# Performance work log

Measured on AMD Instinct MI355X. Metric: run time of the kernel, lower is better.

## Reference

```python
import jax, jax.numpy as jnp
import numpy as np

B, C, H, W, D = 4, 256, 16, 16, 16
N = H * W * D          # 4096 tokens == input_size
HEADS, P = 8, 64       # num_heads, proj_size
EPS_LN, EPS_BN, NEG_SLOPE = 1e-5, 1e-5, 0.01


def setup_inputs() -> dict:
    key = jax.random.key(0)
    ks = jax.random.split(key, 10)
    s = 0.02
    rn = lambda k, shp: (s * jax.random.normal(k, shp)).astype(jnp.float32)
    return {
        "x": jax.random.normal(ks[0], (B, C, H, W, D), jnp.float32),
        "gamma": 1e-6 * jnp.ones((C,), jnp.float32),
        "ln_w": jnp.ones((C,), jnp.float32),
        "ln_b": jnp.zeros((C,), jnp.float32),
        "qkvv_w": rn(ks[1], (4 * C, C)),          # Linear(C, 4C), bias=False
        "ef_w": rn(ks[2], (P, N)),                 # shared E == F projection
        "ef_b": jnp.zeros((P,), jnp.float32),
        "temp": jnp.ones((HEADS, 1, 1), jnp.float32),
        "temp2": jnp.ones((HEADS, 1, 1), jnp.float32),
        "op1_w": rn(ks[3], (C // 2, C)),
        "op1_b": jnp.zeros((C // 2,), jnp.float32),
        "op2_w": rn(ks[4], (C // 2, C)),
        "op2_b": jnp.zeros((C // 2,), jnp.float32),
        "conv1_w": rn(ks[5], (C, C, 3, 3, 3)),     # UnetResBlock convs, bias=False
        "bn1_w": jnp.ones((C,), jnp.float32),
        "bn1_b": jnp.zeros((C,), jnp.float32),
        "conv2_w": rn(ks[6], (C, C, 3, 3, 3)),
        "bn2_w": jnp.ones((C,), jnp.float32),
        "bn2_b": jnp.zeros((C,), jnp.float32),
        "conv8_w": rn(ks[7], (C, C, 1, 1, 1)),     # nn.Conv3d 1x1x1, bias=True
        "conv8_b": jnp.zeros((C,), jnp.float32),
    }


def _l2norm(t):  # torch F.normalize(dim=-1)
    n = jnp.sqrt(jnp.sum(t * t, axis=-1, keepdims=True))
    return t / jnp.maximum(n, 1e-12)


def _conv3d(x, w, pad):
    return jax.lax.conv_general_dilated(
        x, w, window_strides=(1, 1, 1), padding=[(pad, pad)] * 3,
        dimension_numbers=("NCDHW", "OIDHW", "NCDHW"))


def _bn(x, w, b):  # BatchNorm3d, training-mode batch stats, biased var
    mu = jnp.mean(x, axis=(0, 2, 3, 4), keepdims=True)
    var = jnp.mean((x - mu) ** 2, axis=(0, 2, 3, 4), keepdims=True)
    xh = (x - mu) / jnp.sqrt(var + EPS_BN)
    return xh * w[None, :, None, None, None] + b[None, :, None, None, None]


def _lrelu(x):
    return jnp.where(x >= 0, x, NEG_SLOPE * x)


def _epa(xs, qkvv_w, ef_w, ef_b, temp, temp2, op1_w, op1_b, op2_w, op2_b):
    Bq, Nq, Cq = xs.shape
    d = Cq // HEADS
    qkvv = (xs @ qkvv_w.T).reshape(Bq, Nq, 4, HEADS, d)
    qkvv = jnp.transpose(qkvv, (2, 0, 3, 1, 4))         # (4,B,h,N,d)
    q, k, v_ca, v_sa = qkvv[0], qkvv[1], qkvv[2], qkvv[3]
    q = jnp.swapaxes(q, -2, -1)                          # (B,h,d,N)
    k = jnp.swapaxes(k, -2, -1)
    v_ca = jnp.swapaxes(v_ca, -2, -1)
    v_sa = jnp.swapaxes(v_sa, -2, -1)
    k_proj = k @ ef_w.T + ef_b                           # (B,h,d,P)
    v_sa_proj = v_sa @ ef_w.T + ef_b                     # (B,h,d,P)
    qn = _l2norm(q)
    kn = _l2norm(k)
    # channel attention: (B,h,d,d)
    attn_ca = jax.nn.softmax(jnp.einsum("bhdn,bhen->bhde", qn, kn) * temp, axis=-1)
    x_ca = jnp.einsum("bhde,bhen->bhdn", attn_ca, v_ca)  # (B,h,d,N)
    x_ca = jnp.transpose(x_ca, (0, 3, 1, 2)).reshape(Bq, Nq, Cq)
    # spatial attention with projected K/V: (B,h,N,P)
    attn_sa = jax.nn.softmax(jnp.einsum("bhdn,bhdp->bhnp", qn, k_proj) * temp2, axis=-1)
    x_sa = jnp.einsum("bhnp,bhdp->bhnd", attn_sa, v_sa_proj)   # (B,h,N,d)
    # faithful to source: permute(0,3,1,2) then reshape(B,N,C)
    x_sa = jnp.transpose(x_sa, (0, 3, 1, 2)).reshape(Bq, Nq, Cq)
    x_sa = x_sa @ op1_w.T + op1_b
    x_ca = x_ca @ op2_w.T + op2_b
    return jnp.concatenate((x_sa, x_ca), axis=-1)


def reference(x, gamma, ln_w, ln_b, qkvv_w, ef_w, ef_b, temp, temp2,
              op1_w, op1_b, op2_w, op2_b, conv1_w, bn1_w, bn1_b,
              conv2_w, bn2_w, bn2_b, conv8_w, conv8_b):
    Bq, Cq, Hq, Wq, Dq = x.shape
    Nq = Hq * Wq * Dq
    xs = jnp.transpose(x.reshape(Bq, Cq, Nq), (0, 2, 1))       # (B,N,C)
    mu = jnp.mean(xs, axis=-1, keepdims=True)
    var = jnp.mean((xs - mu) ** 2, axis=-1, keepdims=True)
    xn = (xs - mu) / jnp.sqrt(var + EPS_LN) * ln_w + ln_b
    attn = xs + gamma * _epa(xn, qkvv_w, ef_w, ef_b, temp, temp2,
                             op1_w, op1_b, op2_w, op2_b)
    attn_skip = jnp.transpose(attn.reshape(Bq, Hq, Wq, Dq, Cq), (0, 4, 1, 2, 3))
    # UnetResBlock (identity shortcut: same channels, stride 1)
    h1 = _lrelu(_bn(_conv3d(attn_skip, conv1_w, 1), bn1_w, bn1_b))
    h2 = _bn(_conv3d(h1, conv2_w, 1), bn2_w, bn2_b)
    conv_out = _lrelu(h2 + attn_skip)
    # conv8: Dropout3d (identity in eval) + 1x1x1 conv with bias
    c8 = _conv3d(conv_out, conv8_w, 0) + conv8_b[None, :, None, None, None]
    return attn_skip + c8
```

## Files before the change

kernel.cpp:

```cpp
#include <hip/hip_runtime.h>

#define B_ 4
#define C_ 256
#define N_ 4096

typedef unsigned short u16;
typedef __attribute__((ext_vector_type(8))) short short8_t;
typedef __attribute__((ext_vector_type(4))) float f32x4;

__device__ __forceinline__ u16 bf16r(float f) {
  unsigned u = __float_as_uint(f);
  return (u16)((u + 0x7FFFu + ((u >> 16) & 1u)) >> 16);
}
__device__ __forceinline__ float bf2f(u16 u) {
  return __uint_as_float(((unsigned)u) << 16);
}

__device__ __forceinline__ void g2l16(const u16* g, u16* l) {
  __builtin_amdgcn_global_load_lds((const __attribute__((address_space(1))) void*)g,
                                   (__attribute__((address_space(3))) void*)l, 16, 0, 0);
}

__device__ __forceinline__ int f4(int x) { return (x ^ (x >> 2)) & 3; }

__global__ __launch_bounds__(256) void k_pre_ln(const float* __restrict__ x,
                                                const float* __restrict__ ln_w,
                                                const float* __restrict__ ln_b,
                                                const float* __restrict__ qkvv_w,
                                                const float* __restrict__ conv8_w,
                                                const float* __restrict__ op1_w,
                                                const float* __restrict__ op2_w,
                                                const float* __restrict__ ef_w,
                                                const float* __restrict__ conv1_w,
                                                const float* __restrict__ conv2_w,
                                                u16* __restrict__ xnb,
                                                u16* __restrict__ qpack,
                                                u16* __restrict__ w8pack,
                                                u16* __restrict__ oppack,
                                                u16* __restrict__ efpack,
                                                u16* __restrict__ apack1,
                                                u16* __restrict__ apack2,
                                                float* __restrict__ zbuf) {
  __shared__ float tile[32][260];
  __shared__ float s_mu[32], s_rs[32];
  int bid = blockIdx.x, tid = threadIdx.x;
  if (bid < 96) {
    const float* w; u16* dst; int tile_;
    if (bid < 64)      { w = qkvv_w;  dst = qpack;          tile_ = bid; }
    else if (bid < 80) { w = conv8_w; dst = w8pack;         tile_ = bid - 64; }
    else if (bid < 88) { w = op1_w;   dst = oppack;         tile_ = bid - 80; }
    else               { w = op2_w;   dst = oppack + 32768; tile_ = bid - 88; }
    int k0 = tile_ & 7, ot = tile_ >> 3;
    u16* td = dst + (size_t)tile_ * 4096;
    int m = tid >> 1, kb = (tid & 1) * 16, fm = f4(m);
    #pragma unroll
    for (int j = 0; j < 16; ++j) {
      int k = kb + j;
      float v = w[(size_t)(ot * 128 + m) * 256 + k0 * 32 + k];
      td[m * 32 + (((k >> 3) ^ fm) << 3) + (k & 7)] = bf16r(v);
    }
  } else if (bid < 224) {
    int k0 = bid - 96;
    int m = tid & 63, kq = tid >> 6, fm = f4(m);
    u16* td = efpack + (size_t)k0 * 2048;
    #pragma unroll
    for (int kk = 0; kk < 8; ++kk) {
      int k = kq * 8 + kk;
      td[m * 32 + (((k >> 3) ^ fm) << 3) + (k & 7)] = bf16r(ef_w[(size_t)m * 4096 + k0 * 32 + k]);
    }
  } else if (bid < 1088) {
    int t = bid - 224;
    const float* w = (t < 432) ? conv1_w : conv2_w;
    u16* dst = (t < 432) ? apack1 : apack2;
    int tile_ = (t < 432) ? t : t - 432;
    int tap = tile_ % 27; int tmp = tile_ / 27;
    int k0 = tmp & 7; int ot = tmp >> 3;
    u16* td = dst + (size_t)tile_ * 4096;
    int m = tid >> 1, kb = (tid & 1) * 16;
    #pragma unroll
    for (int j = 0; j < 16; ++j) {
      int k = kb + j;
      float v = w[((size_t)(ot * 128 + m) * 256 + k0 * 32 + k) * 27 + tap];
      td[m * 32 + k] = bf16r(v);
    }
  } else if (bid < 1600) {
    int lb = bid - 1088;
    int b = lb >> 7, n0 = (lb & 127) * 32;
    for (int idx = tid; idx < 32 * 256; idx += 256) {
      int nl = idx & 31, c = idx >> 5;
      tile[nl][c] = x[((size_t)(b * C_ + c)) * N_ + n0 + nl];
    }
    __syncthreads();
    int token = tid >> 3, sub = tid & 7;
    float s = 0.f, sq = 0.f;
    for (int j = 0; j < 32; ++j) {
      float v = tile[token][sub + j * 8];
      s += v; sq += v * v;
    }
    for (int o = 1; o < 8; o <<= 1) { s += __shfl_xor(s, o); sq += __shfl_xor(sq, o); }
    if (sub == 0) {
      float mu = s * (1.f / 256.f);
      float var = sq * (1.f / 256.f) - mu * mu;
      s_mu[token] = mu;
      s_rs[token] = rsqrtf(var + 1e-5f);
    }
    __syncthreads();
    int c = tid;
    float lw = ln_w[c], lb2 = ln_b[c];
    for (int k = 0; k < 32; ++k) {
      float v = (tile[k][c] - s_mu[k]) * s_rs[k] * lw + lb2;
      xnb[((size_t)(b * N_ + n0 + k)) * 256 + c] = bf16r(v);
    }
  } else {
    for (int i = tid; i < 3200; i += 256) zbuf[i] = 0.f;
  }
}

__global__ __launch_bounds__(256) void k_gemm(const u16* __restrict__ xnb,
                                              const u16* __restrict__ qpack,
                                              u16* __restrict__ qct,
                                              float* __restrict__ sbuf) {
  __shared__ alignas(16) u16 At[4096];
  __shared__ alignas(16) u16 Bt[4096];
  __shared__ alignas(16) u16 Tt[128 * 136];
  int tid = threadIdx.x, l = tid & 63, w = tid >> 6;
  int wm = w >> 1, wn = w & 1;
  int kg = l >> 4;
  int tok0 = blockIdx.x * 128, oct = blockIdx.y;
  int b = tok0 >> 12;
  int aoff[4], boff[4];
  #pragma unroll
  for (int r = 0; r < 4; ++r) {
    int m = wm * 64 + r * 16 + (l & 15);
    aoff[r] = m * 32 + ((kg ^ f4(m)) << 3);
    int o = wn * 64 + r * 16 + (l & 15);
    boff[r] = o * 32 + ((kg ^ f4(o)) << 3);
  }
  f32x4 acc[4][4];
  #pragma unroll
  for (int r = 0; r < 4; ++r)
    #pragma unroll
    for (int jt = 0; jt < 4; ++jt)
      acc[r][jt] = (f32x4){0.f, 0.f, 0.f, 0.f};
  for (int k0 = 0; k0 < 8; ++k0) {
    __syncthreads();
    #pragma unroll
    for (int it = 0; it < 2; ++it) {
      int slot = it * 256 + tid;
      int row = slot >> 2, cp = slot & 3;
      int cig = cp ^ f4(row);
      g2l16(xnb + ((size_t)(tok0 + row) * 256 + k0 * 32 + cig * 8),
            &At[(it * 256 + (tid & 192)) * 8]);
    }
    const u16* qb = qpack + ((size_t)(oct * 8 + k0) << 12);
    #pragma unroll
    for (int it = 0; it < 2; ++it)
      g2l16(qb + (it * 256 + tid) * 8, &Bt[(it * 256 + (tid & 192)) * 8]);
    __syncthreads();
    short8_t av[4], bv[4];
    #pragma unroll
    for (int r = 0; r < 4; ++r) av[r] = *(const short8_t*)&At[aoff[r]];
    #pragma unroll
    for (int jt = 0; jt < 4; ++jt) bv[jt] = *(const short8_t*)&Bt[boff[jt]];
    #pragma unroll
    for (int r = 0; r < 4; ++r)
      #pragma unroll
      for (int jt = 0; jt < 4; ++jt)
        acc[r][jt] = __builtin_amdgcn_mfma_f32_16x16x32_bf16(av[r], bv[jt], acc[r][jt], 0, 0, 0);
  }
  if (oct < 4) {
    #pragma unroll
    for (int jt = 0; jt < 4; ++jt) {
      float ss = 0.f;
      #pragma unroll
      for (int r = 0; r < 4; ++r)
        #pragma unroll
        for (int reg = 0; reg < 4; ++reg)
          ss += acc[r][jt][reg] * acc[r][jt][reg];
      ss += __shfl_xor(ss, 16);
      ss += __shfl_xor(ss, 32);
      if ((l >> 4) == 0) {
        int oc = oct * 128 + wn * 64 + jt * 16 + (l & 15);
        atomicAdd(&sbuf[(oc >> 8) * 1024 + b * 256 + (oc & 255)], ss);
      }
    }
  }
  #pragma unroll
  for (int r = 0; r < 4; ++r) {
    int tokl = wm * 64 + r * 16 + ((l >> 4) << 2);
    #pragma unroll
    for (int jt = 0; jt < 4; ++jt) {
      int ocl = wn * 64 + jt * 16 + (l & 15);
      ushort4 h4;
      h4.x = bf16r(acc[r][jt][0]);
      h4.y = bf16r(acc[r][jt][1]);
      h4.z = bf16r(acc[r][jt][2]);
      h4.w = bf16r(acc[r][jt][3]);
      *(ushort4*)&Tt[ocl * 136 + tokl] = h4;
    }
  }
  __syncthreads();
  int n0 = tok0 & 4095;
  #pragma unroll
  for (int i = 0; i < 8; ++i) {
    int s = i * 256 + tid;
    int row = s >> 4;
    int col = (s & 15) * 8;
    *(int4*)&qct[((size_t)(b * 1024 + oct * 128 + row)) * 4096 + n0 + col] =
        *(const int4*)&Tt[row * 136 + col];
  }
}

__global__ __launch_bounds__(256) void k_kvproj_m(const u16* __restrict__ qct,
                                                  const u16* __restrict__ efp,
                                                  float* __restrict__ kvpart) {
  __shared__ alignas(16) u16 At[16384];
  __shared__ alignas(16) u16 Bt[8192];
  int tid = threadIdx.x, l = tid & 63, w = tid >> 6;
  int mt = blockIdx.x, b = blockIdx.y, kz = blockIdx.z;
  int ccb = (mt < 2) ? (256 + mt * 128) : (768 + (mt - 2) * 128);
  int kg = l >> 4;
  int aoff[2], boff[4];
  #pragma unroll
  for (int r = 0; r < 2; ++r) {
    int m = w * 32 + r * 16 + (l & 15);
    aoff[r] = m * 32 + ((kg ^ f4(m)) << 3);
  }
  #pragma unroll
  for (int jt = 0; jt < 4; ++jt) {
    int o = jt * 16 + (l & 15);
    boff[jt] = o * 32 + ((kg ^ f4(o)) << 3);
  }
  f32x4 acc[2][4];
  #pragma unroll
  for (int r = 0; r < 2; ++r)
    #pragma unroll
    for (int jt = 0; jt < 4; ++jt) acc[r][jt] = (f32x4){0.f, 0.f, 0.f, 0.f};
  for (int k0 = kz * 8; k0 < kz * 8 + 8; ++k0) {
    __syncthreads();
    #pragma unroll
    for (int it = 0; it < 8; ++it) {
      int slot = it * 256 + tid;
      int sub = slot >> 9, r = (slot >> 2) & 127, cp = slot & 3;
      g2l16(qct + ((size_t)(b * 1024 + ccb + r)) * 4096 + k0 * 128 + sub * 32 + ((cp ^ f4(r)) << 3),
            &At[(it * 256 + (tid & 192)) * 8]);
    }
    #pragma unroll
    for (int it = 0; it < 4; ++it) {
      int slot = it * 256 + tid;
      g2l16(efp + (size_t)k0 * 8192 + slot * 8, &Bt[(it * 256 + (tid & 192)) * 8]);
    }
    __syncthreads();
    #pragma unroll
    for (int sub = 0; sub < 4; ++sub) {
      short8_t av[2], bv[4];
      #pragma unroll
      for (int r = 0; r < 2; ++r) av[r] = *(const short8_t*)&At[sub * 4096 + aoff[r]];
      #pragma unroll
      for (int jt = 0; jt < 4; ++jt) bv[jt] = *(const short8_t*)&Bt[sub * 2048 + boff[jt]];
      #pragma unroll
      for (int r = 0; r < 2; ++r)
        #pragma unroll
        for (int jt = 0; jt < 4; ++jt)
          acc[r][jt] = __builtin_amdgcn_mfma_f32_16x16x32_bf16(av[r], bv[jt], acc[r][jt], 0, 0, 0);
    }
  }
  int kv = mt >> 1;
  float* outd = kvpart + (size_t)kv * 524288 + (size_t)kz * 131072;
  #pragma unroll
  for (int r = 0; r < 2; ++r) {
    int cbase = (mt & 1) * 128 + w * 32 + r * 16 + ((l >> 4) << 2);
    #pragma unroll
    for (int jt = 0; jt < 4; ++jt) {
      int p = jt * 16 + (l & 15);
      #pragma unroll
      for (int reg = 0; reg < 4; ++reg) {
        int cc = cbase + reg;
        outd[((size_t)(b * 8 + (cc >> 5))) * 2048 + (cc & 31) * 64 + p] = acc[r][jt][reg];
      }
    }
  }
}

__global__ __launch_bounds__(256) void k_attnca_p(const u16* __restrict__ qct,
                                                  float* __restrict__ Spp) {
  __shared__ u16 Qs[32][520], Ks[32][520];
  int bh = blockIdx.x, ns = blockIdx.y;
  int b = bh >> 3, h = bh & 7;
  int tid = threadIdx.x;
  int n0 = ns * 512;
  for (int idx = tid; idx < 2048; idx += 256) {
    int r = idx >> 6, ch = (idx & 63) * 8;
    *(int4*)&Qs[r][ch] = *(const int4*)&qct[((size_t)(b * 1024 + h * 32 + r)) * 4096 + n0 + ch];
    *(int4*)&Ks[r][ch] = *(const int4*)&qct[((size_t)(b * 1024 + 256 + h * 32 + r)) * 4096 + n0 + ch];
  }
  __syncthreads();
  int r = tid >> 3, sub = tid & 7;
  float a0 = 0.f, a1 = 0.f, a2 = 0.f, a3 = 0.f;
  for (int nb = 0; nb < 512; nb += 8) {
    short8_t q8 = *(const short8_t*)&Qs[r][nb];
    short8_t k0 = *(const short8_t*)&Ks[sub][nb];
    short8_t k1 = *(const short8_t*)&Ks[sub + 8][nb];
    short8_t k2 = *(const short8_t*)&Ks[sub + 16][nb];
    short8_t k3 = *(const short8_t*)&Ks[sub + 24][nb];
    #pragma unroll
    for (int j = 0; j < 8; ++j) {
      float qv = bf2f((u16)q8[j]);
      a0 += qv * bf2f((u16)k0[j]);
      a1 += qv * bf2f((u16)k1[j]);
      a2 += qv * bf2f((u16)k2[j]);
      a3 += qv * bf2f((u16)k3[j]);
    }
  }
  float* sp = Spp + (size_t)ns * 32768 + (size_t)bh * 1024 + r * 32;
  sp[sub] = a0;
  sp[sub + 8] = a1;
  sp[sub + 16] = a2;
  sp[sub + 24] = a3;
}

__global__ __launch_bounds__(256) void k_xca(const u16* __restrict__ qct,
                                             const float* __restrict__ Spp,
                                             const float* __restrict__ sbuf,
                                             const float* __restrict__ temp,
                                             u16* __restrict__ xca_b) {
  __shared__ float A[32][33];
  __shared__ float vt[32][129];
  int n0 = blockIdx.x * 128;
  int h = blockIdx.y, b = blockIdx.z;
  int bh = b * 8 + h;
  int tid = threadIdx.x;
  if (tid < 32) {
    float qiv = 1.f / fmaxf(sqrtf(sbuf[b * 256 + h * 32 + tid]), 1e-12f);
    float tmp = temp[h];
    float vals[32];
    #pragma unroll
    for (int e = 0; e < 32; ++e) vals[e] = 0.f;
    for (int ns = 0; ns < 8; ++ns) {
      const float* sp = Spp + (size_t)ns * 32768 + (size_t)bh * 1024 + tid * 32;
      #pragma unroll
      for (int e4 = 0; e4 < 32; e4 += 4) {
        float4 v4 = *(const float4*)&sp[e4];
        vals[e4] += v4.x; vals[e4 + 1] += v4.y;
        vals[e4 + 2] += v4.z; vals[e4 + 3] += v4.w;
      }
    }
    float mx = -1e30f;
    #pragma unroll
    for (int e = 0; e < 32; ++e) {
      float kiv = 1.f / fmaxf(sqrtf(sbuf[1024 + b * 256 + h * 32 + e]), 1e-12f);
      float s = vals[e] * qiv * kiv * tmp;
      vals[e] = s;
      mx = fmaxf(mx, s);
    }
    float ssum = 0.f;
    #pragma unroll
    for (int e = 0; e < 32; ++e) { vals[e] = __expf(vals[e] - mx); ssum += vals[e]; }
    float is = 1.f / ssum;
    #pragma unroll
    for (int e = 0; e < 32; ++e) A[tid][e] = vals[e] * is;
  }
  int e = tid >> 3, ns = (tid & 7) * 16;
  const u16* src = qct + ((size_t)(b * 1024 + 512 + h * 32 + e)) * 4096 + n0 + ns;
  #pragma unroll
  for (int j4 = 0; j4 < 16; j4 += 4) {
    ushort4 u = *(const ushort4*)&src[j4];
    vt[e][ns + j4] = bf2f(u.x);
    vt[e][ns + j4 + 1] = bf2f(u.y);
    vt[e][ns + j4 + 2] = bf2f(u.z);
    vt[e][ns + j4 + 3] = bf2f(u.w);
  }
  __syncthreads();
  int nl = tid & 127, dg = (tid >> 7) * 16;
  float acc[16] = {};
  for (int ee = 0; ee < 32; ++ee) {
    float v = vt[ee][nl];
    #pragma unroll
    for (int j = 0; j < 16; ++j) acc[j] += A[dg + j][ee] * v;
  }
  u16* outp = xca_b + ((size_t)(b * N_ + n0 + nl)) * 256 + h * 32 + dg;
  #pragma unroll
  for (int j = 0; j < 16; ++j) outp[j] = bf16r(acc[j]);
}

__global__ __launch_bounds__(256) void k_attnsa(const u16* __restrict__ qct,
                                                const float* __restrict__ kvpart,
                                                const float* __restrict__ ef_b,
                                                const float* __restrict__ sbuf,
                                                const float* __restrict__ temp2,
                                                u16* __restrict__ xsa_b) {
  __shared__ float kp[32][64], vp[32][64], qi[32];
  __shared__ u16 qt[32][260];
  __shared__ float ot[32][257];
  int bx = blockIdx.x;
  int h = blockIdx.y, b = blockIdx.z;
  int bh = b * 8 + h;
  int tid = threadIdx.x;
  for (int idx = tid; idx < 2048; idx += 256) {
    float bias = ef_b[idx & 63];
    float kpv = bias, vpv = bias;
    size_t base = (size_t)bh * 2048 + idx;
    #pragma unroll
    for (int kz = 0; kz < 4; ++kz) {
      kpv += kvpart[(size_t)kz * 131072 + base];
      vpv += kvpart[524288 + (size_t)kz * 131072 + base];
    }
    kp[idx >> 6][idx & 63] = kpv;
    vp[idx >> 6][idx & 63] = vpv;
  }
  if (tid < 32) qi[tid] = 1.f / fmaxf(sqrtf(sbuf[b * 256 + h * 32 + tid]), 1e-12f);
  {
    int row = tid >> 3, ch = (tid & 7) * 32;
    const u16* src = qct + ((size_t)(b * 1024 + h * 32 + row)) * 4096 + bx * 256 + ch;
    *(int4*)&qt[row][ch] = *(const int4*)&src[0];
    *(int4*)&qt[row][ch + 8] = *(const int4*)&src[8];
    *(int4*)&qt[row][ch + 16] = *(const int4*)&src[16];
    *(int4*)&qt[row][ch + 24] = *(const int4*)&src[24];
  }
  __syncthreads();
  float q[32];
  #pragma unroll
  for (int d = 0; d < 32; ++d) q[d] = bf2f(qt[d][tid]) * qi[d];
  float t2 = temp2[h];
  float l[64];
  #pragma unroll
  for (int p = 0; p < 64; ++p) {
    float s = 0;
    #pragma unroll
    for (int d = 0; d < 32; ++d) s += q[d] * kp[d][p];
    l[p] = s * t2;
  }
  float m = -1e30f;
  #pragma unroll
  for (int p = 0; p < 64; ++p) m = fmaxf(m, l[p]);
  float ssum = 0;
  #pragma unroll
  for (int p = 0; p < 64; ++p) { l[p] = __expf(l[p] - m); ssum += l[p]; }
  float is = 1.f / ssum;
  float o[32] = {};
  #pragma unroll
  for (int p = 0; p < 64; ++p) {
    float wv = l[p] * is;
    #pragma unroll
    for (int d = 0; d < 32; ++d) o[d] += wv * vp[d][p];
  }
  #pragma unroll
  for (int d = 0; d < 32; ++d) ot[d][tid] = o[d];
  __syncthreads();
  #pragma unroll
  for (int i = 0; i < 4; ++i) {
    int s = i * 256 + tid;
    int d = s >> 5;
    int c0 = (s & 31) * 8;
    ushort4 u0, u1;
    u0.x = bf16r(ot[d][c0]);     u0.y = bf16r(ot[d][c0 + 1]);
    u0.z = bf16r(ot[d][c0 + 2]); u0.w = bf16r(ot[d][c0 + 3]);
    u1.x = bf16r(ot[d][c0 + 4]); u1.y = bf16r(ot[d][c0 + 5]);
    u1.z = bf16r(ot[d][c0 + 6]); u1.w = bf16r(ot[d][c0 + 7]);
    u16* dst = xsa_b + (size_t)b * N_ * 256 + (size_t)(d * 128 + h * 16 + bx) * 256 + c0;
    *(ushort4*)&dst[0] = u0;
    *(ushort4*)&dst[4] = u1;
  }
}

__global__ __launch_bounds__(256) void k_opcatm(const u16* __restrict__ xsa_b,
                                                const u16* __restrict__ xca_b,
                                                const float* __restrict__ x,
                                                const float* __restrict__ gamma,
                                                const u16* __restrict__ oppack,
                                                const float* __restrict__ op1_b,
                                                const float* __restrict__ op2_b,
                                                u16* __restrict__ attn_skip,
                                                u16* __restrict__ xt1) {
  __shared__ alignas(16) u16 At[4096];
  __shared__ alignas(16) u16 Bt[4096];
  __shared__ alignas(16) float Ttf[128 * 133];
  __shared__ alignas(16) u16 rb[128 * 136];
  int tid = threadIdx.x, l = tid & 63, w = tid >> 6;
  int wm = w >> 1, wn = w & 1;
  int kg = l >> 4;
  int tok0 = blockIdx.x * 128, oct = blockIdx.y;
  int b = tok0 >> 12;
  const u16* src = oct ? xca_b : xsa_b;
  int aoff[4], boff[4];
  #pragma unroll
  for (int r = 0; r < 4; ++r) {
    int m = wm * 64 + r * 16 + (l & 15);
    aoff[r] = m * 32 + ((kg ^ f4(m)) << 3);
    int o = wn * 64 + r * 16 + (l & 15);
    boff[r] = o * 32 + ((kg ^ f4(o)) << 3);
  }
  f32x4 acc[4][4];
  #pragma unroll
  for (int r = 0; r < 4; ++r)
    #pragma unroll
    for (int jt = 0; jt < 4; ++jt)
      acc[r][jt] = (f32x4){0.f, 0.f, 0.f, 0.f};
  for (int k0 = 0; k0 < 8; ++k0) {
    __syncthreads();
    #pragma unroll
    for (int it = 0; it < 2; ++it) {
      int slot = it * 256 + tid;
      int row = slot >> 2, cp = slot & 3;
      int cig = cp ^ f4(row);
      g2l16(src + ((size_t)(tok0 + row) * 256 + k0 * 32 + cig * 8),
            &At[(it * 256 + (tid & 192)) * 8]);
    }
    const u16* qb = oppack + ((size_t)(oct * 8 + k0) << 12);
    #pragma unroll
    for (int it = 0; it < 2; ++it)
      g2l16(qb + (it * 256 + tid) * 8, &Bt[(it * 256 + (tid & 192)) * 8]);
    __syncthreads();
    short8_t av[4], bv[4];
    #pragma unroll
    for (int r = 0; r < 4; ++r) av[r] = *(const short8_t*)&At[aoff[r]];
    #pragma unroll
    for (int jt = 0; jt < 4; ++jt) bv[jt] = *(const short8_t*)&Bt[boff[jt]];
    #pragma unroll
    for (int r = 0; r < 4; ++r)
      #pragma unroll
      for (int jt = 0; jt < 4; ++jt)
        acc[r][jt] = __builtin_amdgcn_mfma_f32_16x16x32_bf16(av[r], bv[jt], acc[r][jt], 0, 0, 0);
  }
  #pragma unroll
  for (int r = 0; r < 4; ++r) {
    int tokl = wm * 64 + r * 16 + ((l >> 4) << 2);
    #pragma unroll
    for (int jt = 0; jt < 4; ++jt) {
      int ocl = wn * 64 + jt * 16 + (l & 15);
      float* tp = &Ttf[ocl * 133 + tokl];
      tp[0] = acc[r][jt][0];
      tp[1] = acc[r][jt][1];
      tp[2] = acc[r][jt][2];
      tp[3] = acc[r][jt][3];
    }
  }
  __syncthreads();
  {
    int n0l = tok0 & 4095;
    #pragma unroll
    for (int i = 0; i < 16; ++i) {
      int s = i * 256 + tid;
      int cl = s >> 5;
      int t4 = (s & 31) * 4;
      int c = oct * 128 + cl;
      float g = gamma[c];
      float bias = oct ? op2_b[cl] : op1_b[cl];
      size_t base = ((size_t)(b * 256 + c)) * 4096 + n0l + t4;
      float4 x4 = *(const float4*)&x[base];
      float* tp = &Ttf[cl * 133 + t4];
      float4 o4;
      o4.x = x4.x + g * (tp[0] + bias);
      o4.y = x4.y + g * (tp[1] + bias);
      o4.z = x4.z + g * (tp[2] + bias);
      o4.w = x4.w + g * (tp[3] + bias);
      ushort4 h4;
      h4.x = bf16r(o4.x); h4.y = bf16r(o4.y);
      h4.z = bf16r(o4.z); h4.w = bf16r(o4.w);
      *(ushort4*)&attn_skip[base] = h4;
      tp[0] = o4.x; tp[1] = o4.y; tp[2] = o4.z; tp[3] = o4.w;
    }
  }
  __syncthreads();
  {
    int cl = tid & 127, th = tid >> 7;
    const float* tp = &Ttf[cl * 133 + th * 64];
    #pragma unroll
    for (int t = 0; t < 64; ++t)
      rb[(th * 64 + t) * 136 + cl] = bf16r(tp[t]);
  }
  __syncthreads();
  {
    int n0l = tok0 & 4095;
    #pragma unroll
    for (int i = 0; i < 8; ++i) {
      int s = i * 256 + tid;
      int row = s >> 4;
      int c0 = (s & 15) * 8;
      *(int4*)&xt1[((size_t)(b * N_ + n0l + row)) * 256 + oct * 128 + c0] =
          *(const int4*)&rb[row * 136 + c0];
    }
  }
}

__global__ __launch_bounds__(256, 2) void k_conv3m(const u16* __restrict__ xt,
                                                   const u16* __restrict__ apack,
                                                   const u16* __restrict__ zg,
                                                   u16* __restrict__ out,
                                                   float* __restrict__ bnsum,
                                                   float* __restrict__ bnsq) {
  __shared__ alignas(16) u16 Xs[2][2][8192];
  int tid = threadIdx.x, l = tid & 63, w = tid >> 6;
  int wm = w & 1, ks = w >> 1;
  int kg = l >> 4;
  int bid = blockIdx.x;
  int cot = bid & 1;
  int sb = (bid >> 1) & 63;
  int b = bid >> 7;
  int h0 = ((sb >> 4) & 3) << 2, w0 = ((sb >> 2) & 3) << 2, d0 = (sb & 3) << 2;

  int cellc[4];
  {
    int cl = l & 15;
    int wv = (cl >> 2) & 3, dv = cl & 3;
    #pragma unroll
    for (int jt = 0; jt < 4; ++jt)
      cellc[jt] = (jt + 1) * 168 + (wv + 1) * 28 + kg * 6 + (dv + 1);
  }
  const int alane = (wm * 64 + (l & 15)) * 32 + kg * 8;

  const u16* xp[4];
  unsigned okm = 0;
  #pragma unroll
  for (int i = 0; i < 4; ++i) {
    int slot = i * 256 + tid;
    int hh = slot / 168;
    int r = slot - hh * 168;
    int ww = r / 28;
    int r2 = r - ww * 28;
    int kk = r2 / 6;
    int dd = r2 - kk * 6;
    int gh = h0 + hh - 1, gw = w0 + ww - 1, gd = d0 + dd - 1;
    bool ok = (hh < 6) && (kk < 4) &&
              ((unsigned)gh < 16u) && ((unsigned)gw < 16u) && ((unsigned)gd < 16u);
    xp[i] = ok ? (xt + ((size_t)(b * N_ + gh * 256 + gw * 16 + gd)) * 256 + kk * 8) : zg;
    okm |= ((unsigned)ok) << i;
  }

  f32x4 acc[4][4];
  #pragma unroll
  for (int r = 0; r < 4; ++r)
    #pragma unroll
    for (int jt = 0; jt < 4; ++jt)
      acc[r][jt] = (f32x4){0.f, 0.f, 0.f, 0.f};

  #pragma unroll
  for (int bk = 0; bk < 2; ++bk)
    #pragma unroll
    for (int i = 0; i < 4; ++i) {
      const u16* p = ((okm >> i) & 1) ? (xp[i] + ((bk * 4) << 5)) : zg;
      g2l16(p, &Xs[bk][0][(i * 256 + (tid & 192)) * 8]);
    }
  __syncthreads();

  short8_t av[4][4], bv[3][4];

#define CONV_TAP(t)                                                                   \
  do {                                                                                \
    if ((t) < 24) {                                                                   \
      const int tnA = (t) + 3;                                                        \
      _Pragma("unroll")                                                               \
      for (int r = 0; r < 4; ++r)                                                     \
        av[tnA & 3][r] = *(const short8_t*)(at + tnA * 4096 + r * 512);               \
    }                                                                                 \
    if ((t) < 25) {                                                                   \
      const int tnB = (t) + 2;                                                        \
      const int dh = tnB / 9, rr_ = tnB - dh * 9, dw = rr_ / 3, dd2 = rr_ - dw * 3;   \
      const int OFF = (dh - 1) * 168 + (dw - 1) * 28 + (dd2 - 1);                     \
      _Pragma("unroll")                                                               \
      for (int jt = 0; jt < 4; ++jt)                                                  \
        bv[tnB % 3][jt] = *(const short8_t*)&Xb[(cellc[jt] + OFF) * 8];               \
    }                                                                                 \
    __builtin_amdgcn_s_setprio(1);                                                    \
    _Pragma("unroll")                                                                 \
    for (int r = 0; r < 4; ++r)                                                       \
      _Pragma("unroll")                                                               \
      for (int jt = 0; jt < 4; ++jt)                                                  \
        acc[r][jt] = __builtin_amdgcn_mfma_f32_16x16x32_bf16(av[(t) & 3][r],          \
                         bv[(t) % 3][jt], acc[r][jt], 0, 0, 0);                       \
    __builtin_amdgcn_s_setprio(0);                                                    \
  } while (0)

  #pragma unroll 1
  for (int step = 0; step < 4; ++step) {
    const int cur = step & 1;
    const u16* Xb = &Xs[ks][cur][0];
    const int ci0 = ks * 4 + step;
    const u16* at = apack + ((size_t)((cot * 8 + ci0) * 27)) * 4096 + alane;
    #pragma unroll
    for (int r = 0; r < 4; ++r) av[0][r] = *(const short8_t*)(at + r * 512);
    #pragma unroll
    for (int r = 0; r < 4; ++r) av[1][r] = *(const short8_t*)(at + 4096 + r * 512);
    #pragma unroll
    for (int r = 0; r < 4; ++r) av[2][r] = *(const short8_t*)(at + 8192 + r * 512);
    #pragma unroll
    for (int jt = 0; jt < 4; ++jt) {
      bv[0][jt] = *(const short8_t*)&Xb[(cellc[jt] - 197) * 8];
      bv[1][jt] = *(const short8_t*)&Xb[(cellc[jt] - 196) * 8];
    }
    #pragma unroll
    for (int t = 0; t < 4; ++t) CONV_TAP(t);
    if (step < 3) {
      const int nd = (step + 1) & 1;
      #pragma unroll
      for (int bk = 0; bk < 2; ++bk)
        #pragma unroll
        for (int i = 0; i < 4; ++i) {
          const u16* p = ((okm >> i) & 1) ? (xp[i] + ((bk * 4 + step + 1) << 5)) : zg;
          g2l16(p, &Xs[bk][nd][(i * 256 + (tid & 192)) * 8]);
        }
    }
    #pragma unroll
    for (int t = 4; t < 27; ++t) CONV_TAP(t);
    __syncthreads();
  }
#undef CONV_TAP

  f32x4* red = (f32x4*)&Xs[0][0][0];
  if (ks == 1) {
    #pragma unroll
    for (int r = 0; r < 4; ++r)
      #pragma unroll
      for (int jt = 0; jt < 4; ++jt)
        red[(r * 4 + jt) * 128 + wm * 64 + l] = acc[r][jt];
  }
  __syncthreads();
  if (ks == 0) {
    #pragma unroll
    for (int r = 0; r < 4; ++r)
      #pragma unroll
      for (int jt = 0; jt < 4; ++jt) {
        f32x4 o = red[(r * 4 + jt) * 128 + wm * 64 + l];
        acc[r][jt][0] += o[0]; acc[r][jt][1] += o[1];
        acc[r][jt][2] += o[2]; acc[r][jt][3] += o[3];
      }
    #pragma unroll
    for (int r = 0; r < 4; ++r) {
      int co = cot * 128 + wm * 64 + r * 16 + ((l >> 4) << 2);
      #pragma unroll
      for (int reg = 0; reg < 4; ++reg) {
        float sv = 0.f, qv = 0.f;
        #pragma unroll
        for (int jt = 0; jt < 4; ++jt) {
          float v = acc[r][jt][reg];
          sv += v; qv += v * v;
        }
        #pragma unroll
        for (int o = 1; o < 16; o <<= 1) {
          sv += __shfl_xor(sv, o);
          qv += __shfl_xor(qv, o);
        }
        if ((l & 15) == 0) {
          atomicAdd(&bnsum[co + reg], sv);
          atomicAdd(&bnsq[co + reg], qv);
        }
      }
      #pragma unroll
      for (int jt = 0; jt < 4; ++jt) {
        int c = jt * 16 + (l & 15);
        int n = (h0 + (c >> 4)) * 256 + (w0 + ((c >> 2) & 3)) * 16 + (d0 + (c & 3));
        ushort4 h4;
        h4.x = bf16r(acc[r][jt][0]);
        h4.y = bf16r(acc[r][jt][1]);
        h4.z = bf16r(acc[r][jt][2]);
        h4.w = bf16r(acc[r][jt][3]);
        *(ushort4*)&out[((size_t)(b * N_ + n)) * 256 + co] = h4;
      }
    }
  }
}

__global__ __launch_bounds__(256) void k_bnelt(const u16* __restrict__ src,
                                               const float* __restrict__ bnsum,
                                               const float* __restrict__ bnsq,
                                               const float* __restrict__ w,
                                               const float* __restrict__ bb,
                                               u16* __restrict__ dst) {
  __shared__ float sc[256], sh[256];
  int tid = threadIdx.x;
  float m = bnsum[tid] * (1.f / 16384.f);
  float var = bnsq[tid] * (1.f / 16384.f) - m * m;
  float rstd = rsqrtf(var + 1e-5f);
  float scv = rstd * w[tid];
  sc[tid] = scv;
  sh[tid] = bb[tid] - m * scv;
  __syncthreads();
  size_t base = (size_t)blockIdx.x * 64 * 256;
  #pragma unroll
  for (int i = 0; i < 8; ++i) {
    int s = i * 256 + tid;
    int c0 = (s & 31) * 8;
    size_t off = base + (size_t)(s >> 5) * 256 + c0;
    int4 v4 = *(const int4*)&src[off];
    u16* pu = (u16*)&v4;
    #pragma unroll
    for (int j = 0; j < 8; ++j) {
      float v = bf2f(pu[j]) * sc[c0 + j] + sh[c0 + j];
      pu[j] = bf16r(v >= 0.f ? v : 0.01f * v);
    }
    *(int4*)&dst[off] = v4;
  }
}

__global__ __launch_bounds__(256) void k_bn2fuse(const u16* __restrict__ c2o,
                                                 const u16* __restrict__ askip,
                                                 const float* __restrict__ bnsum,
                                                 const float* __restrict__ bnsq,
                                                 const float* __restrict__ bnw,
                                                 const float* __restrict__ bnb,
                                                 u16* __restrict__ cvo) {
  __shared__ float sc[256], sh[256];
  __shared__ float at_[32][260];
  int n0 = blockIdx.x * 32, b = blockIdx.y, tid = threadIdx.x;
  float m = bnsum[tid] * (1.f / 16384.f);
  float var = bnsq[tid] * (1.f / 16384.f) - m * m;
  float rstd = rsqrtf(var + 1e-5f);
  float scv = rstd * bnw[tid];
  sc[tid] = scv;
  sh[tid] = bnb[tid] - m * scv;
  #pragma unroll
  for (int i = 0; i < 8; ++i) {
    int s = i * 256 + tid;
    int c = s >> 3;
    int t4 = (s & 7) * 4;
    ushort4 a4 = *(const ushort4*)&askip[((size_t)(b * 256 + c)) * 4096 + n0 + t4];
    at_[t4 + 0][c] = bf2f(a4.x);
    at_[t4 + 1][c] = bf2f(a4.y);
    at_[t4 + 2][c] = bf2f(a4.z);
    at_[t4 + 3][c] = bf2f(a4.w);
  }
  __syncthreads();
  #pragma unroll
  for (int i = 0; i < 4; ++i) {
    int s = i * 256 + tid;
    int row = s >> 5, c0 = (s & 31) * 8;
    size_t off = ((size_t)(b * N_ + n0 + row)) * 256 + c0;
    int4 v4 = *(const int4*)&c2o[off];
    u16* pu = (u16*)&v4;
    #pragma unroll
    for (int j = 0; j < 8; ++j) {
      int c = c0 + j;
      float v = bf2f(pu[j]) * sc[c] + sh[c] + at_[row][c];
      pu[j] = bf16r(v >= 0.f ? v : 0.01f * v);
    }
    *(int4*)&cvo[off] = v4;
  }
}

__global__ __launch_bounds__(256) void k_conv8m(const u16* __restrict__ cvo,
                                                const u16* __restrict__ w8p,
                                                const float* __restrict__ b8,
                                                const u16* __restrict__ skip,
                                                float* __restrict__ out) {
  __shared__ alignas(16) u16 At[4096];
  __shared__ alignas(16) u16 Bt[4096];
  __shared__ alignas(16) float Ts[128 * 132];
  int tid = threadIdx.x, l = tid & 63, w = tid >> 6;
  int wm = w >> 1, wn = w & 1;
  int kg = l >> 4;
  int tok0 = blockIdx.x * 128, oct = blockIdx.y;
  int b = tok0 >> 12;
  int aoff[4], boff[4];
  #pragma unroll
  for (int r = 0; r < 4; ++r) {
    int m = wm * 64 + r * 16 + (l & 15);
    aoff[r] = m * 32 + ((kg ^ f4(m)) << 3);
    int o = wn * 64 + r * 16 + (l & 15);
    boff[r] = o * 32 + ((kg ^ f4(o)) << 3);
  }
  f32x4 acc[4][4];
  #pragma unroll
  for (int r = 0; r < 4; ++r)
    #pragma unroll
    for (int jt = 0; jt < 4; ++jt)
      acc[r][jt] = (f32x4){0.f, 0.f, 0.f, 0.f};
  for (int k0 = 0; k0 < 8; ++k0) {
    __syncthreads();
    #pragma unroll
    for (int it = 0; it < 2; ++it) {
      int slot = it * 256 + tid;
      int row = slot >> 2, cp = slot & 3;
      int cig = cp ^ f4(row);
      g2l16(cvo + ((size_t)(tok0 + row) * 256 + k0 * 32 + cig * 8),
            &At[(it * 256 + (tid & 192)) * 8]);
    }
    const u16* qb = w8p + ((size_t)(oct * 8 + k0) << 12);
    #pragma unroll
    for (int it = 0; it < 2; ++it)
      g2l16(qb + (it * 256 + tid) * 8, &Bt[(it * 256 + (tid & 192)) * 8]);
    __syncthreads();
    short8_t av[4], bv[4];
    #pragma unroll
    for (int r = 0; r < 4; ++r) av[r] = *(const short8_t*)&At[aoff[r]];
    #pragma unroll
    for (int jt = 0; jt < 4; ++jt) bv[jt] = *(const short8_t*)&Bt[boff[jt]];
    #pragma unroll
    for (int r = 0; r < 4; ++r)
      #pragma unroll
      for (int jt = 0; jt < 4; ++jt)
        acc[r][jt] = __builtin_amdgcn_mfma_f32_16x16x32_bf16(av[r], bv[jt], acc[r][jt], 0, 0, 0);
  }
  #pragma unroll
  for (int r = 0; r < 4; ++r) {
    int tokl = wm * 64 + r * 16 + ((l >> 4) << 2);
    #pragma unroll
    for (int jt = 0; jt < 4; ++jt) {
      int ocl = wn * 64 + jt * 16 + (l & 15);
      *(float4*)&Ts[ocl * 132 + tokl] =
          (float4){acc[r][jt][0], acc[r][jt][1], acc[r][jt][2], acc[r][jt][3]};
    }
  }
  __syncthreads();
  int n0l = tok0 & 4095;
  #pragma unroll
  for (int i = 0; i < 16; ++i) {
    int s = i * 256 + tid;
    int row = s >> 5;
    int c4 = (s & 31) * 4;
    int oc = oct * 128 + row;
    size_t base = ((size_t)(b * 256 + oc)) * 4096 + n0l + c4;
    ushort4 s4 = *(const ushort4*)&skip[base];
    float bias = b8[oc];
    const float* tp = &Ts[row * 132 + c4];
    float4 o4;
    o4.x = bf2f(s4.x) + bias + tp[0];
    o4.y = bf2f(s4.y) + bias + tp[1];
    o4.z = bf2f(s4.z) + bias + tp[2];
    o4.w = bf2f(s4.w) + bias + tp[3];
    *(float4*)&out[base] = o4;
  }
}

extern "C" void kernel_launch(void* const* d_in, const int* in_sizes, int n_in,
                              void* d_out, int out_size, void* d_ws, size_t ws_size,
                              hipStream_t stream) {
  const float* x       = (const float*)d_in[0];
  const float* gamma   = (const float*)d_in[1];
  const float* ln_w    = (const float*)d_in[2];
  const float* ln_b    = (const float*)d_in[3];
  const float* qkvv_w  = (const float*)d_in[4];
  const float* ef_w    = (const float*)d_in[5];
  const float* ef_b    = (const float*)d_in[6];
  const float* temp    = (const float*)d_in[7];
  const float* temp2   = (const float*)d_in[8];
  const float* op1_w   = (const float*)d_in[9];
  const float* op1_b   = (const float*)d_in[10];
  const float* op2_w   = (const float*)d_in[11];
  const float* op2_b   = (const float*)d_in[12];
  const float* conv1_w = (const float*)d_in[13];
  const float* bn1_w   = (const float*)d_in[14];
  const float* bn1_b   = (const float*)d_in[15];
  const float* conv2_w = (const float*)d_in[16];
  const float* bn2_w   = (const float*)d_in[17];
  const float* bn2_b   = (const float*)d_in[18];
  const float* conv8_w = (const float*)d_in[19];
  const float* conv8_b = (const float*)d_in[20];

  float* ws = (float*)d_ws;
  const size_t M1 = 1u << 20;
  u16*   askip  = (u16*)ws;
  u16*   apack1 = (u16*)(ws + 8 * M1);
  u16*   apack2 = (u16*)(ws + 10 * M1);
  u16*   xt1    = (u16*)(ws + 16 * M1);
  u16*   xnb    = (u16*)(ws + 18 * M1);
  u16*   xsa_b  = (u16*)(ws + 18 * M1);
  float* Spp    = ws + 19 * M1;
  float* kvpart = ws + 20 * M1;
  u16*   xca_b  = (u16*)(ws + 22 * M1);
  u16*   cvo    = (u16*)(ws + 22 * M1);
  u16*   qct    = (u16*)(ws + 24 * M1);
  u16*   c1o    = (u16*)(ws + 26 * M1);
  u16*   ht     = (u16*)(ws + 28 * M1);
  u16*   c2o    = (u16*)(ws + 30 * M1);
  float* sm     = ws + 32 * M1;
  float* sbuf   = sm;
  float* bnacc  = sm + 2048;
  float* zgu_f  = sm + 3072;
  u16*   zgu    = (u16*)zgu_f;
  u16*   qpack  = (u16*)(sm + 3200);
  u16*   efpack = (u16*)(sm + 3200 + 131072);
  u16*   w8pack = (u16*)(sm + 3200 + 262144);
  u16*   oppack = (u16*)(sm + 3200 + 294912);

  k_pre_ln<<<dim3(1601), 256, 0, stream>>>(x, ln_w, ln_b, qkvv_w, conv8_w, op1_w, op2_w,
                                           ef_w, conv1_w, conv2_w,
                                           xnb, qpack, w8pack, oppack, efpack,
                                           apack1, apack2, sm);
  k_gemm<<<dim3(128, 8), 256, 0, stream>>>(xnb, qpack, qct, sbuf);
  k_kvproj_m<<<dim3(4, 4, 4), 256, 0, stream>>>(qct, efpack, kvpart);
  k_attnca_p<<<dim3(32, 8), 256, 0, stream>>>(qct, Spp);
  k_xca<<<dim3(32, 8, 4), 256, 0, stream>>>(qct, Spp, sbuf, temp, xca_b);
  k_attnsa<<<dim3(16, 8, 4), 256, 0, stream>>>(qct, kvpart, ef_b, sbuf, temp2, xsa_b);
  k_opcatm<<<dim3(128, 2), 256, 0, stream>>>(xsa_b, xca_b, x, gamma, oppack, op1_b, op2_b, askip, xt1);
  k_conv3m<<<dim3(512), 256, 0, stream>>>(xt1, apack1, zgu, c1o, bnacc, bnacc + 256);
  k_bnelt<<<dim3(256), 256, 0, stream>>>(c1o, bnacc, bnacc + 256, bn1_w, bn1_b, ht);
  k_conv3m<<<dim3(512), 256, 0, stream>>>(ht, apack2, zgu, c2o, bnacc + 512, bnacc + 768);
  k_bn2fuse<<<dim3(128, 4), 256, 0, stream>>>(c2o, askip, bnacc + 512, bnacc + 768, bn2_w, bn2_b, cvo);
  k_conv8m<<<dim3(128, 2), 256, 0, stream>>>(cvo, w8pack, conv8_b, askip, (float*)d_out);
}
```

Baseline: 321.9 us.

## Use MFMA for channel-attention scores and halve kvproj tile for more blocks

The channel-attention score kernel switches from scalar bf16 dot products staged through LDS to MFMA 16x16x32 instructions that read operands straight from global memory. Each wave covers a 128-token slice, and the four wave partials are reduced through LDS before a vectorized store. Separately, the K/V projection kernel halves its M tile from 128 to 64 channels and doubles the grid, which raises parallelism and cuts LDS use per block. In exchange, each block loads the E/F tile twice as often in total across the grid.

```diff
diff --git a/kernel.cpp b/kernel.cpp
--- a/kernel.cpp
+++ b/kernel.cpp
@@ -214,34 +214,32 @@
 __global__ __launch_bounds__(256) void k_kvproj_m(const u16* __restrict__ qct,
                                                   const u16* __restrict__ efp,
                                                   float* __restrict__ kvpart) {
-  __shared__ alignas(16) u16 At[16384];
+  __shared__ alignas(16) u16 At[8192];
   __shared__ alignas(16) u16 Bt[8192];
   int tid = threadIdx.x, l = tid & 63, w = tid >> 6;
   int mt = blockIdx.x, b = blockIdx.y, kz = blockIdx.z;
-  int ccb = (mt < 2) ? (256 + mt * 128) : (768 + (mt - 2) * 128);
+  int kv = mt >> 2, q = mt & 3;
+  int ccb = (kv ? 768 : 256) + q * 64;
   int kg = l >> 4;
-  int aoff[2], boff[4];
-  #pragma unroll
-  for (int r = 0; r < 2; ++r) {
-    int m = w * 32 + r * 16 + (l & 15);
-    aoff[r] = m * 32 + ((kg ^ f4(m)) << 3);
+  int aoff, boff[4];
+  {
+    int m = w * 16 + (l & 15);
+    aoff = m * 32 + ((kg ^ f4(m)) << 3);
   }
   #pragma unroll
   for (int jt = 0; jt < 4; ++jt) {
     int o = jt * 16 + (l & 15);
     boff[jt] = o * 32 + ((kg ^ f4(o)) << 3);
   }
-  f32x4 acc[2][4];
-  #pragma unroll
-  for (int r = 0; r < 2; ++r)
-    #pragma unroll
-    for (int jt = 0; jt < 4; ++jt) acc[r][jt] = (f32x4){0.f, 0.f, 0.f, 0.f};
+  f32x4 acc[4];
+  #pragma unroll
+  for (int jt = 0; jt < 4; ++jt) acc[jt] = (f32x4){0.f, 0.f, 0.f, 0.f};
   for (int k0 = kz * 8; k0 < kz * 8 + 8; ++k0) {
     __syncthreads();
     #pragma unroll
-    for (int it = 0; it < 8; ++it) {
+    for (int it = 0; it < 4; ++it) {
       int slot = it * 256 + tid;
-      int sub = slot >> 9, r = (slot >> 2) & 127, cp = slot & 3;
+      int sub = slot >> 8, r = (slot >> 2) & 63, cp = slot & 3;
       g2l16(qct + ((size_t)(b * 1024 + ccb + r)) * 4096 + k0 * 128 + sub * 32 + ((cp ^ f4(r)) << 3),
             &At[(it * 256 + (tid & 192)) * 8]);
     }
@@ -253,70 +251,73 @@
     __syncthreads();
     #pragma unroll
     for (int sub = 0; sub < 4; ++sub) {
-      short8_t av[2], bv[4];
-      #pragma unroll
-      for (int r = 0; r < 2; ++r) av[r] = *(const short8_t*)&At[sub * 4096 + aoff[r]];
+      short8_t av = *(const short8_t*)&At[sub * 2048 + aoff];
+      short8_t bv[4];
       #pragma unroll
       for (int jt = 0; jt < 4; ++jt) bv[jt] = *(const short8_t*)&Bt[sub * 2048 + boff[jt]];
       #pragma unroll
-      for (int r = 0; r < 2; ++r)
-        #pragma unroll
-        for (int jt = 0; jt < 4; ++jt)
-          acc[r][jt] = __builtin_amdgcn_mfma_f32_16x16x32_bf16(av[r], bv[jt], acc[r][jt], 0, 0, 0);
-    }
-  }
-  int kv = mt >> 1;
+      for (int jt = 0; jt < 4; ++jt)
+        acc[jt] = __builtin_amdgcn_mfma_f32_16x16x32_bf16(av, bv[jt], acc[jt], 0, 0, 0);
+    }
+  }
   float* outd = kvpart + (size_t)kv * 524288 + (size_t)kz * 131072;
   #pragma unroll
-  for (int r = 0; r < 2; ++r) {
-    int cbase = (mt & 1) * 128 + w * 32 + r * 16 + ((l >> 4) << 2);
-    #pragma unroll
-    for (int jt = 0; jt < 4; ++jt) {
-      int p = jt * 16 + (l & 15);
-      #pragma unroll
-      for (int reg = 0; reg < 4; ++reg) {
-        int cc = cbase + reg;
-        outd[((size_t)(b * 8 + (cc >> 5))) * 2048 + (cc & 31) * 64 + p] = acc[r][jt][reg];
-      }
+  for (int jt = 0; jt < 4; ++jt) {
+    int p = jt * 16 + (l & 15);
+    #pragma unroll
+    for (int reg = 0; reg < 4; ++reg) {
+      int cc = q * 64 + w * 16 + (kg << 2) + reg;
+      outd[((size_t)(b * 8 + (cc >> 5))) * 2048 + (cc & 31) * 64 + p] = acc[jt][reg];
     }
   }
 }
 
 __global__ __launch_bounds__(256) void k_attnca_p(const u16* __restrict__ qct,
                                                   float* __restrict__ Spp) {
-  __shared__ u16 Qs[32][520], Ks[32][520];
+  __shared__ float ld[4224];
   int bh = blockIdx.x, ns = blockIdx.y;
   int b = bh >> 3, h = bh & 7;
-  int tid = threadIdx.x;
-  int n0 = ns * 512;
-  for (int idx = tid; idx < 2048; idx += 256) {
-    int r = idx >> 6, ch = (idx & 63) * 8;
-    *(int4*)&Qs[r][ch] = *(const int4*)&qct[((size_t)(b * 1024 + h * 32 + r)) * 4096 + n0 + ch];
-    *(int4*)&Ks[r][ch] = *(const int4*)&qct[((size_t)(b * 1024 + 256 + h * 32 + r)) * 4096 + n0 + ch];
-  }
-  __syncthreads();
-  int r = tid >> 3, sub = tid & 7;
-  float a0 = 0.f, a1 = 0.f, a2 = 0.f, a3 = 0.f;
-  for (int nb = 0; nb < 512; nb += 8) {
-    short8_t q8 = *(const short8_t*)&Qs[r][nb];
-    short8_t k0 = *(const short8_t*)&Ks[sub][nb];
-    short8_t k1 = *(const short8_t*)&Ks[sub + 8][nb];
-    short8_t k2 = *(const short8_t*)&Ks[sub + 16][nb];
-    short8_t k3 = *(const short8_t*)&Ks[sub + 24][nb];
-    #pragma unroll
-    for (int j = 0; j < 8; ++j) {
-      float qv = bf2f((u16)q8[j]);
-      a0 += qv * bf2f((u16)k0[j]);
-      a1 += qv * bf2f((u16)k1[j]);
-      a2 += qv * bf2f((u16)k2[j]);
-      a3 += qv * bf2f((u16)k3[j]);
-    }
-  }
-  float* sp = Spp + (size_t)ns * 32768 + (size_t)bh * 1024 + r * 32;
-  sp[sub] = a0;
-  sp[sub + 8] = a1;
-  sp[sub + 16] = a2;
-  sp[sub + 24] = a3;
+  int tid = threadIdx.x, l = tid & 63, w = tid >> 6;
+  int row = l & 15, kg = l >> 4;
+  int n0 = ns * 512 + w * 128;
+  const u16* qbase = qct + ((size_t)(b * 1024 + h * 32 + row)) * 4096 + n0 + kg * 8;
+  const u16* kbase = qct + ((size_t)(b * 1024 + 256 + h * 32 + row)) * 4096 + n0 + kg * 8;
+  f32x4 acc[2][2];
+  #pragma unroll
+  for (int qt = 0; qt < 2; ++qt)
+    #pragma unroll
+    for (int et = 0; et < 2; ++et) acc[qt][et] = (f32x4){0.f, 0.f, 0.f, 0.f};
+  #pragma unroll
+  for (int ki = 0; ki < 4; ++ki) {
+    short8_t aq0 = *(const short8_t*)(qbase + ki * 32);
+    short8_t aq1 = *(const short8_t*)(qbase + (size_t)16 * 4096 + ki * 32);
+    short8_t bk0 = *(const short8_t*)(kbase + ki * 32);
+    short8_t bk1 = *(const short8_t*)(kbase + (size_t)16 * 4096 + ki * 32);
+    acc[0][0] = __builtin_amdgcn_mfma_f32_16x16x32_bf16(aq0, bk0, acc[0][0], 0, 0, 0);
+    acc[0][1] = __builtin_amdgcn_mfma_f32_16x16x32_bf16(aq0, bk1, acc[0][1], 0, 0, 0);
+    acc[1][0] = __builtin_amdgcn_mfma_f32_16x16x32_bf16(aq1, bk0, acc[1][0], 0, 0, 0);
+    acc[1][1] = __builtin_amdgcn_mfma_f32_16x16x32_bf16(aq1, bk1, acc[1][1], 0, 0, 0);
+  }
+  #pragma unroll
+  for (int qt = 0; qt < 2; ++qt)
+    #pragma unroll
+    for (int et = 0; et < 2; ++et)
+      #pragma unroll
+      for (int r = 0; r < 4; ++r)
+        ld[w * 1056 + (qt * 16 + kg * 4 + r) * 33 + et * 16 + row] = acc[qt][et][r];
+  __syncthreads();
+  {
+    int idx4 = tid * 4;
+    int qq = idx4 >> 5, e0 = idx4 & 31;
+    float s0 = 0.f, s1 = 0.f, s2 = 0.f, s3 = 0.f;
+    #pragma unroll
+    for (int ww = 0; ww < 4; ++ww) {
+      const float* p = &ld[ww * 1056 + qq * 33 + e0];
+      s0 += p[0]; s1 += p[1]; s2 += p[2]; s3 += p[3];
+    }
+    float4 o4 = {s0, s1, s2, s3};
+    *(float4*)&Spp[(size_t)ns * 32768 + (size_t)bh * 1024 + idx4] = o4;
+  }
 }
 
 __global__ __launch_bounds__(256) void k_xca(const u16* __restrict__ qct,
@@ -977,7 +978,7 @@
                                            xnb, qpack, w8pack, oppack, efpack,
                                            apack1, apack2, sm);
   k_gemm<<<dim3(128, 8), 256, 0, stream>>>(xnb, qpack, qct, sbuf);
-  k_kvproj_m<<<dim3(4, 4, 4), 256, 0, stream>>>(qct, efpack, kvpart);
+  k_kvproj_m<<<dim3(8, 4, 4), 256, 0, stream>>>(qct, efpack, kvpart);
   k_attnca_p<<<dim3(32, 8), 256, 0, stream>>>(qct, Spp);
   k_xca<<<dim3(32, 8, 4), 256, 0, stream>>>(qct, Spp, sbuf, temp, xca_b);
   k_attnsa<<<dim3(16, 8, 4), 256, 0, stream>>>(qct, kvpart, ef_b, sbuf, temp2, xsa_b);
```

Result: faster. 307.7 us (-4.4%).
